# Performance work log

Hardware: AMD Instinct MI355X
Metric: run time of the kernel (lower is better)

The kernel has to match this reference:

```python
import jax, jax.numpy as jnp
import numpy as np

B, DIN, E, FACTOR, STEPS, NH = 2048, 1024, 1024, 16, 3, 8
DH = E // NH
EPS = 1e-5


def layernorm(x, g, b):
    m = x.mean(-1, keepdims=True)
    v = ((x - m) ** 2).mean(-1, keepdims=True)
    return (x - m) / jnp.sqrt(v + EPS) * g + b


def setup_inputs() -> dict:
    key = jax.random.key(0)
    ks = iter(jax.random.split(key, 32))
    r = lambda shape, s=0.02: jax.random.normal(next(ks), shape, dtype=jnp.float32) * s
    F = E * FACTOR
    return {
        "image_feat": jax.random.normal(next(ks), (B, DIN), dtype=jnp.float32),
        "text_feat": jax.random.normal(next(ks), (B, DIN), dtype=jnp.float32),
        # fusion block
        "fc1_w": r((F, DIN)), "fc1_b": jnp.zeros((F,), jnp.float32),
        "fc2_w": r((F, DIN)), "fc2_b": jnp.zeros((F,), jnp.float32),
        "fc3_w": r((E, F)), "fc3_b": jnp.zeros((E,), jnp.float32),
        "ln_g": jnp.ones((E,), jnp.float32), "ln_b": jnp.zeros((E,), jnp.float32),
        # per-step MHA + FFN + norms, stacked over STEPS
        "Wqkv": r((STEPS, 3 * E, E)), "bqkv": jnp.zeros((STEPS, 3 * E), jnp.float32),
        "Wo": r((STEPS, E, E)), "bo": jnp.zeros((STEPS, E), jnp.float32),
        "W1": r((STEPS, E, E)), "b1": jnp.zeros((STEPS, E), jnp.float32),
        "W2": r((STEPS, E, E)), "b2": jnp.zeros((STEPS, E), jnp.float32),
        "n1_g": jnp.ones((STEPS, E), jnp.float32), "n1_b": jnp.zeros((STEPS, E), jnp.float32),
        "n2_g": jnp.ones((STEPS, E), jnp.float32), "n2_b": jnp.zeros((STEPS, E), jnp.float32),
        # output projection
        "Wout": r((DIN, E)), "bout": jnp.zeros((DIN,), jnp.float32),
    }


def mha_step(q, ctx, Wqkv, bqkv, Wo, bo):
    # q: [B,E] (query len 1), ctx: [B,L,E]
    Wq, Wk, Wv = Wqkv[:E], Wqkv[E:2 * E], Wqkv[2 * E:]
    bq, bk, bv = bqkv[:E], bqkv[E:2 * E], bqkv[2 * E:]
    L = ctx.shape[1]
    qh = (q @ Wq.T + bq).reshape(B, NH, DH)
    kh = (ctx @ Wk.T + bk).reshape(B, L, NH, DH)
    vh = (ctx @ Wv.T + bv).reshape(B, L, NH, DH)
    scores = jnp.einsum("bhd,blhd->bhl", qh, kh) / jnp.sqrt(jnp.float32(DH))
    attn = jax.nn.softmax(scores, axis=-1)
    out = jnp.einsum("bhl,blhd->bhd", attn, vh).reshape(B, E)
    return out @ Wo.T + bo


def reference(image_feat, text_feat, fc1_w, fc1_b, fc2_w, fc2_b, fc3_w, fc3_b,
              ln_g, ln_b, Wqkv, bqkv, Wo, bo, W1, b1, W2, b2,
              n1_g, n1_b, n2_g, n2_b, Wout, bout):
    # fusion block (dropout = identity in eval)
    fused = (image_feat @ fc1_w.T + fc1_b) * (text_feat @ fc2_w.T + fc2_b)
    fused = layernorm(fused @ fc3_w.T + fc3_b, ln_g, ln_b)  # [B,E]
    ctx = fused[:, None, :]  # [B,1,E]
    x = fused
    for i in range(STEPS):
        attn = mha_step(x, ctx, Wqkv[i], bqkv[i], Wo[i], bo[i])
        x = x + layernorm(attn, n1_g[i], n1_b[i])
        ffn = jax.nn.relu(x @ W1[i].T + b1[i]) @ W2[i].T + b2[i]
        x = x + layernorm(ffn, n2_g[i], n2_b[i])
        ctx = jnp.concatenate([ctx, x[:, None, :]], axis=1)
    final_output = x @ Wout.T + bout  # [B,DIN]
    return final_output, ctx
```

## Files before the change

### kernel.cpp

```cpp
#include <hip/hip_runtime.h>

#define TB 256

typedef __attribute__((ext_vector_type(8))) short short8;
typedef __attribute__((ext_vector_type(4))) float f32x4;
typedef unsigned short u16;

constexpr int B_  = 2048;
constexpr int DIN = 1024;
constexpr int E   = 1024;
constexpr int F   = 16384;
constexpr int E3  = 3072;
constexpr int CH  = 4096;

struct Ptr8 { void* p[8]; };

__device__ __forceinline__ u16 f2bf(float f) {
  union { float f; unsigned u; } v; v.f = f;
  unsigned r = v.u + 0x7fffu + ((v.u >> 16) & 1u);
  return (u16)(r >> 16);
}
__device__ __forceinline__ float bf2f(u16 u) {
  union { unsigned u; float f; } v; v.u = ((unsigned)u) << 16;
  return v.f;
}

__device__ __forceinline__ void gload16(const void* g, void* l) {
  __builtin_amdgcn_global_load_lds(
      (const __attribute__((address_space(1))) void*)g,
      (__attribute__((address_space(3))) void*)l, 16, 0, 0);
}

__device__ __forceinline__ void tile_xy(int& tx, int& ty) {
  int gx = gridDim.x;
  int nwg = gx * gridDim.y;
  int wg = blockIdx.y * gx + blockIdx.x;
  if ((nwg & 7) == 0) wg = (wg & 7) * (nwg >> 3) + (wg >> 3);
  tx = wg % gx; ty = wg / gx;
}

__device__ __forceinline__ int swz16(int o) {
  return o ^ (((o >> 7) & 7) << 4);
}

__global__ __launch_bounds__(256) void cvt_kernel(const float* __restrict__ s,
                                                  u16* __restrict__ d, int n) {
  int i = (blockIdx.x * 256 + threadIdx.x) * 4;
  if (i >= n) return;
  float4 v = *(const float4*)&s[i];
  ushort4 o;
  o.x = f2bf(v.x); o.y = f2bf(v.y); o.z = f2bf(v.z); o.w = f2bf(v.w);
  *(ushort4*)&d[i] = o;
}

__global__ __launch_bounds__(256) void fill_kernel(float* p, int n, float v) {
  int i = blockIdx.x * 256 + threadIdx.x;
  if (i < n) p[i] = v;
}

__global__ __launch_bounds__(256) void relu_multi_kernel(
    Ptr8 ys, int ny, const float* __restrict__ bias, u16* __restrict__ out) {
  size_t i = ((size_t)blockIdx.x * 256 + threadIdx.x) * 4;
  int col = (int)(i & 1023);
  float4 b = *(const float4*)&bias[col];
  float a0 = b.x, a1 = b.y, a2 = b.z, a3 = b.w;
  for (int j = 0; j < ny; ++j) {
    float4 z = *(const float4*)&((const float*)ys.p[j])[i];
    a0 += z.x; a1 += z.y; a2 += z.z; a3 += z.w;
  }
  ushort4 o;
  o.x = f2bf(a0 > 0.f ? a0 : 0.f);
  o.y = f2bf(a1 > 0.f ? a1 : 0.f);
  o.z = f2bf(a2 > 0.f ? a2 : 0.f);
  o.w = f2bf(a3 > 0.f ? a3 : 0.f);
  *(ushort4*)&out[i] = o;
}

__global__ __launch_bounds__(256) void combine_out_kernel(
    Ptr8 ys, int ny, const float* __restrict__ bias, float* __restrict__ out) {
  size_t i = ((size_t)blockIdx.x * 256 + threadIdx.x) * 4;
  int col = (int)(i & 1023);
  float4 b = *(const float4*)&bias[col];
  float a0 = b.x, a1 = b.y, a2 = b.z, a3 = b.w;
  for (int j = 0; j < ny; ++j) {
    float4 z = *(const float4*)&((const float*)ys.p[j])[i];
    a0 += z.x; a1 += z.y; a2 += z.z; a3 += z.w;
  }
  out[i] = a0; out[i + 1] = a1; out[i + 2] = a2; out[i + 3] = a3;
}

template <int EPI>
__global__ __launch_bounds__(512, 2) void gemm256(
    const u16* __restrict__ A, int sA,
    const u16* __restrict__ Bw, int sB,
    const float* __restrict__ bias, const u16* __restrict__ gate,
    void* __restrict__ Out, Ptr8 pouts, int ldOut, int ksz) {
  __shared__ __align__(16) char smem[131072];
  const int tid = threadIdx.x, lane = tid & 63, w = tid >> 6;
  const int wm = w >> 2, wn = w & 3;
  int tx, ty; tile_xy(tx, ty);
  const int m0 = tx * 256, n0 = ty * 256;
  const int k0 = blockIdx.z * ksz;
  const int nt = ksz >> 6;
  const int lr = lane & 15;

  f32x4 acc[8][4] = {};

  auto stage = [&](const u16* __restrict__ G, int gs, int gr0, int kk, int tb, int j) {
    int P = j * 8192 + w * 1024 + lane * 16;
    int L = swz16(P);
    int row = L >> 7, colb = L & 127;
    gload16(G + (size_t)(gr0 + row) * gs + kk + (colb >> 1),
            &smem[tb + j * 8192 + w * 1024]);
  };
  auto rdA = [&](int tb, int mf, int kh) -> short8 {
    int Lo = (wm * 128 + mf * 16 + lr) * 128 + kh * 64 + (lane >> 4) * 16;
    return *(const short8*)&smem[tb + swz16(Lo)];
  };
  auto rdB = [&](int tb, int nf, int kh) -> short8 {
    int Lo = (wn * 64 + nf * 16 + lr) * 128 + kh * 64 + (lane >> 4) * 16;
    return *(const short8*)&smem[tb + swz16(Lo)];
  };

#pragma unroll
  for (int j = 0; j < 4; ++j) stage(A, sA, m0, k0, 0, j);
#pragma unroll
  for (int j = 0; j < 4; ++j) stage(Bw, sB, n0, k0, 65536, j);
  asm volatile("s_waitcnt vmcnt(0)" ::: "memory");
  __builtin_amdgcn_sched_barrier(0);
  __builtin_amdgcn_s_barrier();

  int cur = 0;
  for (int t = 0; t < nt; ++t) {
    const int sa = cur * 32768;
    const int sb = 65536 + cur * 32768;
    if (t + 1 < nt) {
      const int sa2 = (cur ^ 1) * 32768;
      const int sb2 = 65536 + (cur ^ 1) * 32768;
#pragma unroll
      for (int j = 0; j < 4; ++j) stage(A, sA, m0, k0 + (t + 1) * 64, sa2, j);
#pragma unroll
      for (int j = 0; j < 4; ++j) stage(Bw, sB, n0, k0 + (t + 1) * 64, sb2, j);
    }
    short8 bfr[4][2], afr[4][2];
#pragma unroll
    for (int nf = 0; nf < 4; ++nf)
#pragma unroll
      for (int kh = 0; kh < 2; ++kh) bfr[nf][kh] = rdB(sb, nf, kh);
#pragma unroll
    for (int mf = 0; mf < 4; ++mf)
#pragma unroll
      for (int kh = 0; kh < 2; ++kh) afr[mf][kh] = rdA(sa, mf, kh);
    __builtin_amdgcn_s_setprio(1);
#pragma unroll
    for (int mf = 0; mf < 4; ++mf)
#pragma unroll
      for (int nf = 0; nf < 4; ++nf)
#pragma unroll
        for (int kh = 0; kh < 2; ++kh)
          acc[mf][nf] = __builtin_amdgcn_mfma_f32_16x16x32_bf16(
              afr[mf][kh], bfr[nf][kh], acc[mf][nf], 0, 0, 0);
    __builtin_amdgcn_s_setprio(0);
#pragma unroll
    for (int mf = 0; mf < 4; ++mf)
#pragma unroll
      for (int kh = 0; kh < 2; ++kh) afr[mf][kh] = rdA(sa, 4 + mf, kh);
    __builtin_amdgcn_s_setprio(1);
#pragma unroll
    for (int mf = 0; mf < 4; ++mf)
#pragma unroll
      for (int nf = 0; nf < 4; ++nf)
#pragma unroll
        for (int kh = 0; kh < 2; ++kh)
          acc[4 + mf][nf] = __builtin_amdgcn_mfma_f32_16x16x32_bf16(
              afr[mf][kh], bfr[nf][kh], acc[4 + mf][nf], 0, 0, 0);
    __builtin_amdgcn_s_setprio(0);
    if (t + 1 < nt) {
      asm volatile("s_waitcnt vmcnt(0)" ::: "memory");
      __builtin_amdgcn_sched_barrier(0);
      __builtin_amdgcn_s_barrier();
    }
    cur ^= 1;
  }

  float* Pf = (EPI == 0) ? (float*)pouts.p[blockIdx.z] : nullptr;
  const int rb = (lane >> 4) * 4;
#pragma unroll
  for (int mf = 0; mf < 8; ++mf) {
#pragma unroll
    for (int nf = 0; nf < 4; ++nf) {
      int row0 = m0 + wm * 128 + mf * 16 + rb;
      int col  = n0 + wn * 64 + nf * 16 + lr;
      float bv = (EPI == 0 || bias == nullptr) ? 0.f : bias[col];
#pragma unroll
      for (int r = 0; r < 4; ++r) {
        float v = acc[mf][nf][r] + bv;
        size_t idx = (size_t)(row0 + r) * ldOut + col;
        if (EPI == 0)      Pf[idx] = v;
        else if (EPI == 4) ((u16*)Out)[idx] = f2bf(v * bf2f(gate[idx]));
        else               ((u16*)Out)[idx] = f2bf(v);
      }
    }
  }
}

template <int EPI>
__global__ __launch_bounds__(TB) void gemm_bt(
    const u16* __restrict__ A, int sA,
    const u16* __restrict__ Bw, int sB,
    const float* __restrict__ bias, Ptr8 outs,
    int ldOut, int Kext, int ksz) {
  __shared__ u16 As[128 * 32];
  __shared__ u16 Bs[128 * 32];
  const int tid = threadIdx.x, lane = tid & 63, w = tid >> 6;
  const int wr = w >> 1, wc = w & 1;
  int tx, ty; tile_xy(tx, ty);
  const int m0 = tx * 128, n0 = ty * 128;
  const int k0 = blockIdx.z * ksz;
  const int kend = min(k0 + ksz, Kext);

  f32x4 acc[4][4] = {};
  const int lr = lane & 15, lk = (lane >> 4) * 8;

  for (int kk = k0; kk < kend; kk += 32) {
#pragma unroll
    for (int is = 0; is < 2; ++is) {
      int c = is * 256 + tid;
      int r = c >> 2, kc = (c & 3) << 3;
      size_t lb = (size_t)(is * 256 + w * 64) * 8;
      gload16(A  + (size_t)(m0 + r) * sA + kk + kc, &As[lb]);
      gload16(Bw + (size_t)(n0 + r) * sB + kk + kc, &Bs[lb]);
    }
    __syncthreads();
    short8 af[4], bfv[4];
#pragma unroll
    for (int m = 0; m < 4; ++m)
      af[m] = *(const short8*)&As[(wr * 64 + m * 16 + lr) * 32 + lk];
#pragma unroll
    for (int n = 0; n < 4; ++n)
      bfv[n] = *(const short8*)&Bs[(wc * 64 + n * 16 + lr) * 32 + lk];
#pragma unroll
    for (int m = 0; m < 4; ++m)
#pragma unroll
      for (int n = 0; n < 4; ++n)
        acc[m][n] = __builtin_amdgcn_mfma_f32_16x16x32_bf16(af[m], bfv[n], acc[m][n], 0, 0, 0);
    __syncthreads();
  }

  float* Of = (float*)outs.p[EPI == 0 ? blockIdx.z : 0];
  const int rbase = (lane >> 4) * 4;
#pragma unroll
  for (int m = 0; m < 4; ++m) {
#pragma unroll
    for (int n = 0; n < 4; ++n) {
      int row0 = m0 + wr * 64 + m * 16 + rbase;
      int col  = n0 + wc * 64 + n * 16 + lr;
      float bv = (bias == nullptr) ? 0.f : bias[col];
#pragma unroll
      for (int r = 0; r < 4; ++r) {
        float v = acc[m][n][r] + bv;
        size_t idx = (size_t)(row0 + r) * ldOut + col;
        if (EPI == 0) Of[idx] = v;
        else          ((u16*)Of)[idx] = f2bf(v);
      }
    }
  }
}

template <int EPI>
__global__ __launch_bounds__(TB) void gemm_wf32(
    const u16* __restrict__ A, int sA,
    const float* __restrict__ Bw, int sB,
    const float* __restrict__ bias, void* __restrict__ Out, int ldOut,
    int Kext, int ksz) {
  __shared__ u16 As[128 * 32];
  __shared__ u16 Bs[128 * 32];
  const int tid = threadIdx.x, lane = tid & 63, w = tid >> 6;
  const int wr = w >> 1, wc = w & 1;
  int tx, ty; tile_xy(tx, ty);
  const int m0 = tx * 128, n0 = ty * 128;
  const int k0 = blockIdx.z * ksz;
  const int kend = min(k0 + ksz, Kext);

  f32x4 acc[4][4] = {};
  const int lr = lane & 15, lk = (lane >> 4) * 8;

  for (int kk = k0; kk < kend; kk += 32) {
#pragma unroll
    for (int is = 0; is < 2; ++is) {
      int c = is * 256 + tid;
      int r = c >> 2, kc = (c & 3) << 3;
      gload16(A + (size_t)(m0 + r) * sA + kk + kc,
              &As[(size_t)(is * 256 + w * 64) * 8]);
    }
#pragma unroll
    for (int p = 0; p < 4; ++p) {
      int t = tid + p * 256;
      int r = t >> 3, c4 = (t & 7) << 2;
      float4 v = *(const float4*)&Bw[(size_t)(n0 + r) * sB + kk + c4];
      ushort4 o;
      o.x = f2bf(v.x); o.y = f2bf(v.y); o.z = f2bf(v.z); o.w = f2bf(v.w);
      *(ushort4*)&Bs[r * 32 + c4] = o;
    }
    __syncthreads();
    short8 af[4], bfv[4];
#pragma unroll
    for (int m = 0; m < 4; ++m)
      af[m] = *(const short8*)&As[(wr * 64 + m * 16 + lr) * 32 + lk];
#pragma unroll
    for (int n = 0; n < 4; ++n)
      bfv[n] = *(const short8*)&Bs[(wc * 64 + n * 16 + lr) * 32 + lk];
#pragma unroll
    for (int m = 0; m < 4; ++m)
#pragma unroll
      for (int n = 0; n < 4; ++n)
        acc[m][n] = __builtin_amdgcn_mfma_f32_16x16x32_bf16(af[m], bfv[n], acc[m][n], 0, 0, 0);
    __syncthreads();
  }

  const int rbase = (lane >> 4) * 4;
#pragma unroll
  for (int m = 0; m < 4; ++m) {
#pragma unroll
    for (int n = 0; n < 4; ++n) {
      int row0 = m0 + wr * 64 + m * 16 + rbase;
      int col  = n0 + wc * 64 + n * 16 + lr;
      float bv = (EPI == 3 || bias == nullptr) ? 0.f : bias[col];
#pragma unroll
      for (int r = 0; r < 4; ++r) {
        float v = acc[m][n][r] + bv;
        size_t idx = (size_t)(row0 + r) * ldOut + col;
        if (EPI == 0)      ((float*)Out)[idx] = v;
        else if (EPI == 1) ((u16*)Out)[idx] = f2bf(v);
        else if (EPI == 2) ((u16*)Out)[idx] = f2bf(v > 0.f ? v : 0.f);
        else               atomicAdd((float*)Out + idx, v);
      }
    }
  }
}

__global__ __launch_bounds__(TB) void gemm_dual_wf32(
    const u16* __restrict__ A1, const u16* __restrict__ A2, int sA,
    const float* __restrict__ B1, const float* __restrict__ B2, int sB,
    const float* __restrict__ bias1, const float* __restrict__ bias2,
    u16* __restrict__ Out, int ldOut, int K) {
  __shared__ u16 As1[128 * 32];
  __shared__ u16 As2[128 * 32];
  __shared__ u16 Bs1[128 * 32];
  __shared__ u16 Bs2[128 * 32];
  const int tid = threadIdx.x, lane = tid & 63, w = tid >> 6;
  const int wr = w >> 1, wc = w & 1;
  int tx, ty; tile_xy(tx, ty);
  const int m0 = tx * 128, n0 = ty * 128;

  f32x4 acc1[4][4] = {};
  f32x4 acc2[4][4] = {};
  const int lr = lane & 15, lk = (lane >> 4) * 8;

  for (int kk = 0; kk < K; kk += 32) {
#pragma unroll
    for (int is = 0; is < 2; ++is) {
      int c = is * 256 + tid;
      int r = c >> 2, kc = (c & 3) << 3;
      size_t lb = (size_t)(is * 256 + w * 64) * 8;
      gload16(A1 + (size_t)(m0 + r) * sA + kk + kc, &As1[lb]);
      gload16(A2 + (size_t)(m0 + r) * sA + kk + kc, &As2[lb]);
    }
#pragma unroll
    for (int p = 0; p < 4; ++p) {
      int t = tid + p * 256;
      int r = t >> 3, c4 = (t & 7) << 2;
      float4 v1 = *(const float4*)&B1[(size_t)(n0 + r) * sB + kk + c4];
      float4 v2 = *(const float4*)&B2[(size_t)(n0 + r) * sB + kk + c4];
      ushort4 o1, o2;
      o1.x = f2bf(v1.x); o1.y = f2bf(v1.y); o1.z = f2bf(v1.z); o1.w = f2bf(v1.w);
      o2.x = f2bf(v2.x); o2.y = f2bf(v2.y); o2.z = f2bf(v2.z); o2.w = f2bf(v2.w);
      *(ushort4*)&Bs1[r * 32 + c4] = o1;
      *(ushort4*)&Bs2[r * 32 + c4] = o2;
    }
    __syncthreads();
    short8 a1[4], a2[4], b1v[4], b2v[4];
#pragma unroll
    for (int m = 0; m < 4; ++m) {
      a1[m] = *(const short8*)&As1[(wr * 64 + m * 16 + lr) * 32 + lk];
      a2[m] = *(const short8*)&As2[(wr * 64 + m * 16 + lr) * 32 + lk];
    }
#pragma unroll
    for (int n = 0; n < 4; ++n) {
      b1v[n] = *(const short8*)&Bs1[(wc * 64 + n * 16 + lr) * 32 + lk];
      b2v[n] = *(const short8*)&Bs2[(wc * 64 + n * 16 + lr) * 32 + lk];
    }
#pragma unroll
    for (int m = 0; m < 4; ++m)
#pragma unroll
      for (int n = 0; n < 4; ++n) {
        acc1[m][n] = __builtin_amdgcn_mfma_f32_16x16x32_bf16(a1[m], b1v[n], acc1[m][n], 0, 0, 0);
        acc2[m][n] = __builtin_amdgcn_mfma_f32_16x16x32_bf16(a2[m], b2v[n], acc2[m][n], 0, 0, 0);
      }
    __syncthreads();
  }

  const int rbase = (lane >> 4) * 4;
#pragma unroll
  for (int m = 0; m < 4; ++m) {
#pragma unroll
    for (int n = 0; n < 4; ++n) {
      int row0 = m0 + wr * 64 + m * 16 + rbase;
      int col  = n0 + wc * 64 + n * 16 + lr;
      float bv1 = bias1[col], bv2 = bias2[col];
#pragma unroll
      for (int r = 0; r < 4; ++r) {
        float v = (acc1[m][n][r] + bv1) * (acc2[m][n][r] + bv2);
        Out[(size_t)(row0 + r) * ldOut + col] = f2bf(v);
      }
    }
  }
}

template <int MODE>
__global__ __launch_bounds__(256) void resln_kernel(
    Ptr8 ys, int ny, const float* __restrict__ preb,
    const float* __restrict__ g, const float* __restrict__ bp,
    float* __restrict__ x, u16* __restrict__ xb,
    float* __restrict__ ctxo, int ctxRow) {
  const int r = blockIdx.x, tid = threadIdx.x;
  const size_t base = (size_t)r * 1024 + tid * 4;
  float y[4] = {0.f, 0.f, 0.f, 0.f};
  for (int j = 0; j < ny; ++j) {
    float4 z = *(const float4*)&((const float*)ys.p[j])[base];
    y[0] += z.x; y[1] += z.y; y[2] += z.z; y[3] += z.w;
  }
  if (preb != nullptr) {
    float4 p4 = *(const float4*)&preb[tid * 4];
    y[0] += p4.x; y[1] += p4.y; y[2] += p4.z; y[3] += p4.w;
  }
  float s = y[0] + y[1] + y[2] + y[3];
  float q = y[0] * y[0] + y[1] * y[1] + y[2] * y[2] + y[3] * y[3];
  __shared__ float red[8];
  for (int o = 32; o; o >>= 1) { s += __shfl_xor(s, o); q += __shfl_xor(q, o); }
  int wv = tid >> 6;
  if ((tid & 63) == 0) { red[wv] = s; red[4 + wv] = q; }
  __syncthreads();
  s = red[0] + red[1] + red[2] + red[3];
  q = red[4] + red[5] + red[6] + red[7];
  float mean = s * (1.f / 1024.f);
  float var  = q * (1.f / 1024.f) - mean * mean;
  float rs   = rsqrtf(var + 1e-5f);
  float4 g4 = *(const float4*)&g[tid * 4];
  float4 b4 = *(const float4*)&bp[tid * 4];
  float gg[4] = {g4.x, g4.y, g4.z, g4.w};
  float bb[4] = {b4.x, b4.y, b4.z, b4.w};
  float xv[4];
#pragma unroll
  for (int j = 0; j < 4; ++j) {
    float val = (y[j] - mean) * rs * gg[j] + bb[j];
    xv[j] = (MODE == 0) ? val : x[base + j] + val;
  }
  *(float4*)&x[base] = make_float4(xv[0], xv[1], xv[2], xv[3]);
  ushort4 xo;
  xo.x = f2bf(xv[0]); xo.y = f2bf(xv[1]); xo.z = f2bf(xv[2]); xo.w = f2bf(xv[3]);
  *(ushort4*)&xb[base] = xo;
  if (MODE != 1) {
    size_t cb = ((size_t)r * 4 + ctxRow) * 1024 + tid * 4;
    *(float4*)&ctxo[cb] = make_float4(xv[0], xv[1], xv[2], xv[3]);
  }
}

__global__ __launch_bounds__(64) void attn_kernel(const u16* __restrict__ qkv,
                                                  u16* __restrict__ out, int L) {
  const int b = blockIdx.x >> 3, h = blockIdx.x & 7;
  const int lane = threadIdx.x;
  const size_t qoff = ((size_t)(L - 1) * B_ + b) * E3 + h * 128;
  float q0 = bf2f(qkv[qoff + lane]);
  float q1 = bf2f(qkv[qoff + 64 + lane]);
  float sc[3];
  for (int l = 0; l < L; ++l) {
    size_t kb = ((size_t)l * B_ + b) * E3 + 1024 + h * 128;
    float p = q0 * bf2f(qkv[kb + lane]) + q1 * bf2f(qkv[kb + 64 + lane]);
    for (int o = 32; o; o >>= 1) p += __shfl_xor(p, o);
    sc[l] = p * 0.08838834764831843f;
  }
  float m = sc[0];
  for (int l = 1; l < L; ++l) m = fmaxf(m, sc[l]);
  float wsum = 0.f, wgt[3];
  for (int l = 0; l < L; ++l) { wgt[l] = expf(sc[l] - m); wsum += wgt[l]; }
  float inv = 1.f / wsum;
  float o0 = 0.f, o1 = 0.f;
  for (int l = 0; l < L; ++l) {
    size_t vb = ((size_t)l * B_ + b) * E3 + 2048 + h * 128;
    o0 += wgt[l] * bf2f(qkv[vb + lane]);
    o1 += wgt[l] * bf2f(qkv[vb + 64 + lane]);
  }
  out[(size_t)b * 1024 + h * 128 + lane]      = f2bf(o0 * inv);
  out[(size_t)b * 1024 + h * 128 + 64 + lane] = f2bf(o1 * inv);
}

extern "C" void kernel_launch(void* const* d_in, const int* in_sizes, int n_in,
                              void* d_out, int out_size, void* d_ws, size_t ws_size,
                              hipStream_t stream) {
  (void)in_sizes; (void)n_in;
  const float* image = (const float*)d_in[0];
  const float* text  = (const float*)d_in[1];
  const float* fc1_w = (const float*)d_in[2];
  const float* fc1_b = (const float*)d_in[3];
  const float* fc2_w = (const float*)d_in[4];
  const float* fc2_b = (const float*)d_in[5];
  const float* fc3_w = (const float*)d_in[6];
  const float* fc3_b = (const float*)d_in[7];
  const float* ln_g  = (const float*)d_in[8];
  const float* ln_b  = (const float*)d_in[9];
  const float* Wqkv  = (const float*)d_in[10];
  const float* bqkv  = (const float*)d_in[11];
  const float* Wo    = (const float*)d_in[12];
  const float* bo    = (const float*)d_in[13];
  const float* W1    = (const float*)d_in[14];
  const float* b1    = (const float*)d_in[15];
  const float* W2    = (const float*)d_in[16];
  const float* b2    = (const float*)d_in[17];
  const float* n1_g  = (const float*)d_in[18];
  const float* n1_b  = (const float*)d_in[19];
  const float* n2_g  = (const float*)d_in[20];
  const float* n2_b  = (const float*)d_in[21];
  const float* WoutW = (const float*)d_in[22];
  const float* boutW = (const float*)d_in[23];

  float* outF   = (float*)d_out;
  float* ctxOut = outF + (size_t)B_ * DIN;
  char* ws = (char*)d_ws;

  auto cvt = [&](const float* s, u16* d, size_t n) {
    cvt_kernel<<<dim3((unsigned)((n + 1023) / 1024)), 256, 0, stream>>>(s, d, (int)n);
  };

  const size_t NEED_A = 232783872;
  if (ws_size >= NEED_A) {
    size_t off = 0;
    auto carve = [&](size_t bytes) -> char* {
      char* p = ws + off; off += (bytes + 255) & ~(size_t)255; return p;
    };
    u16* imgB  = (u16*)carve((size_t)B_ * DIN * 2);
    u16* txtB  = (u16*)carve((size_t)B_ * DIN * 2);
    u16* fc1B  = (u16*)carve((size_t)F * DIN * 2);
    u16* fc2B  = (u16*)carve((size_t)F * DIN * 2);
    u16* fc3B  = (u16*)carve((size_t)E * F * 2);
    u16* WqkvB = (u16*)carve((size_t)3 * E3 * E * 2);
    u16* WoB   = (u16*)carve((size_t)3 * E * E * 2);
    u16* W1B   = (u16*)carve((size_t)3 * E * E * 2);
    u16* W2B   = (u16*)carve((size_t)3 * E * E * 2);
    u16* WoutB = (u16*)carve((size_t)DIN * E * 2);
    char* U    = carve((size_t)B_ * F * 2);
    float* xF  = (float*)carve((size_t)B_ * E * 4);
    float* hF  = (float*)carve((size_t)B_ * E * 4);
    u16* fusedB = (u16*)U;
    u16* qkvB   = (u16*)(U);
    u16* ctxB   = (u16*)(U + 37748736);
    u16* attnB  = (u16*)(U + 37748736 + 16777216);
    u16* h1B    = (u16*)(U + 37748736 + 16777216 + 4194304);
    u16* xbB    = (u16*)(U + 37748736 + 16777216 + 8388608);
    float* PA = (float*)fc1B;
    float* PB = (float*)(fc1B + 4194304);
    float* PC = (float*)(fc1B + 8388608);
    float* PD = (float*)(fc1B + 12582912);
    float* PE = (float*)fc2B;
    float* PF = (float*)(fc2B + 4194304);
    float* PG = (float*)(fc2B + 8388608);

    cvt(image, imgB, (size_t)B_ * DIN);
    cvt(text,  txtB, (size_t)B_ * DIN);
    cvt(fc1_w, fc1B, (size_t)F * DIN);
    cvt(fc2_w, fc2B, (size_t)F * DIN);
    cvt(fc3_w, fc3B, (size_t)E * F);
    cvt(Wqkv,  WqkvB, (size_t)3 * E3 * E);
    cvt(Wo,    WoB,   (size_t)3 * E * E);
    cvt(W1,    W1B,   (size_t)3 * E * E);
    cvt(W2,    W2B,   (size_t)3 * E * E);
    cvt(WoutW, WoutB, (size_t)DIN * E);

    Ptr8 dumb{};
    gemm256<1><<<dim3(B_ / 256, F / 256), 512, 0, stream>>>(
        txtB, DIN, fc2B, DIN, fc2_b, nullptr, fusedB, dumb, F, DIN);
    gemm256<4><<<dim3(B_ / 256, F / 256), 512, 0, stream>>>(
        imgB, DIN, fc1B, DIN, fc1_b, fusedB, fusedB, dumb, F, DIN);
    Ptr8 p8f{{xF, hF, PA, PB, PC, PD, PE, PF}};
    gemm256<0><<<dim3(B_ / 256, E / 256, 8), 512, 0, stream>>>(
        fusedB, F, fc3B, F, nullptr, nullptr, nullptr, p8f, E, F / 8);
    resln_kernel<0><<<B_, 256, 0, stream>>>(
        p8f, 8, fc3_b, ln_g, ln_b, xF, ctxB, ctxOut, 0);

    Ptr8 p8l{{hF, outF, PA, PB, PC, PD, PE, PF}};
    for (int i = 0; i < 3; ++i) {
      int L = i + 1;
      Ptr8 q1{{qkvB, nullptr, nullptr, nullptr, nullptr, nullptr, nullptr, nullptr}};
      gemm_bt<1><<<dim3(L * B_ / 128, E3 / 128), TB, 0, stream>>>(
          ctxB, E, WqkvB + (size_t)i * E3 * E, E, bqkv + (size_t)i * E3,
          q1, E3, E, E);
      attn_kernel<<<B_ * 8, 64, 0, stream>>>(qkvB, attnB, L);
      gemm_bt<0><<<dim3(B_ / 128, E / 128, 8), TB, 0, stream>>>(
          attnB, E, WoB + (size_t)i * E * E, E, nullptr, p8l, E, E, E / 8);
      resln_kernel<1><<<B_, 256, 0, stream>>>(
          p8l, 8, bo + (size_t)i * E, n1_g + (size_t)i * E, n1_b + (size_t)i * E,
          xF, xbB, nullptr, 0);
      gemm_bt<0><<<dim3(B_ / 128, E / 128, 8), TB, 0, stream>>>(
          xbB, E, W1B + (size_t)i * E * E, E, nullptr, p8l, E, E, E / 8);
      relu_multi_kernel<<<B_ * E / 1024, 256, 0, stream>>>(
          p8l, 8, b1 + (size_t)i * E, h1B);
      gemm_bt<0><<<dim3(B_ / 128, E / 128, 8), TB, 0, stream>>>(
          h1B, E, W2B + (size_t)i * E * E, E, nullptr, p8l, E, E, E / 8);
      resln_kernel<2><<<B_, 256, 0, stream>>>(
          p8l, 8, b2 + (size_t)i * E, n2_g + (size_t)i * E, n2_b + (size_t)i * E,
          xF, ctxB + (size_t)(i + 1) * B_ * E, ctxOut, i + 1);
    }

    Ptr8 pfin{{hF, PA, PB, PC, PD, PE, PF, PG}};
    gemm_bt<0><<<dim3(B_ / 128, DIN / 128, 8), TB, 0, stream>>>(
        ctxB + (size_t)3 * B_ * E, E, WoutB, E, nullptr, pfin, DIN, E, E / 8);
    combine_out_kernel<<<B_ * DIN / 1024, 256, 0, stream>>>(pfin, 8, boutW, outF);
    return;
  }

  size_t off = 0;
  auto carve = [&](size_t bytes) -> char* {
    char* p = ws + off; off += (bytes + 255) & ~(size_t)255; return p;
  };
  u16* imgB   = (u16*)carve((size_t)B_ * DIN * 2);
  u16* txtB   = (u16*)carve((size_t)B_ * DIN * 2);
  u16* fusedC = (u16*)carve((size_t)B_ * CH * 2);
  u16* qkvB   = (u16*)carve((size_t)3 * B_ * E3 * 2);
  u16* ctxB   = (u16*)carve((size_t)4 * B_ * E * 2);
  u16* attnB  = (u16*)carve((size_t)B_ * E * 2);
  u16* h1B    = (u16*)carve((size_t)B_ * E * 2);
  u16* xbB    = (u16*)carve((size_t)B_ * E * 2);
  float* xF   = (float*)carve((size_t)B_ * E * 4);
  float* hF   = (float*)carve((size_t)B_ * E * 4);

  if (off > ws_size) {
    fill_kernel<<<(out_size + 255) / 256, 256, 0, stream>>>(outF, out_size, 12345.0f);
    return;
  }

  cvt(image, imgB, (size_t)B_ * DIN);
  cvt(text,  txtB, (size_t)B_ * DIN);
  hipMemsetAsync(hF, 0, (size_t)B_ * E * 4, stream);

  for (int c = 0; c < F / CH; ++c) {
    gemm_dual_wf32<<<dim3(B_ / 128, CH / 128), TB, 0, stream>>>(
        imgB, txtB, DIN,
        fc1_w + (size_t)c * CH * DIN, fc2_w + (size_t)c * CH * DIN, DIN,
        fc1_b + (size_t)c * CH, fc2_b + (size_t)c * CH, fusedC, CH, DIN);
    gemm_wf32<3><<<dim3(B_ / 128, E / 128, 2), TB, 0, stream>>>(
        fusedC, CH, fc3_w + (size_t)c * CH, F, nullptr, hF, E, CH, CH / 2);
  }
  {
    Ptr8 y1{{hF, nullptr, nullptr, nullptr, nullptr, nullptr, nullptr, nullptr}};
    resln_kernel<0><<<B_, 256, 0, stream>>>(y1, 1, fc3_b, ln_g, ln_b, xF, ctxB, ctxOut, 0);
  }

  for (int i = 0; i < 3; ++i) {
    int L = i + 1;
    gemm_wf32<1><<<dim3(L * B_ / 128, E3 / 128), TB, 0, stream>>>(
        ctxB, E, Wqkv + (size_t)i * E3 * E, E, bqkv + (size_t)i * E3, qkvB, E3, E, E);
    attn_kernel<<<B_ * 8, 64, 0, stream>>>(qkvB, attnB, L);
    gemm_wf32<0><<<dim3(B_ / 128, E / 128), TB, 0, stream>>>(
        attnB, E, Wo + (size_t)i * E * E, E, bo + (size_t)i * E, hF, E, E, E);
    Ptr8 y1{{hF, nullptr, nullptr, nullptr, nullptr, nullptr, nullptr, nullptr}};
    resln_kernel<1><<<B_, 256, 0, stream>>>(
        y1, 1, nullptr, n1_g + (size_t)i * E, n1_b + (size_t)i * E, xF, xbB, nullptr, 0);
    gemm_wf32<2><<<dim3(B_ / 128, E / 128), TB, 0, stream>>>(
        xbB, E, W1 + (size_t)i * E * E, E, b1 + (size_t)i * E, h1B, E, E, E);
    gemm_wf32<0><<<dim3(B_ / 128, E / 128), TB, 0, stream>>>(
        h1B, E, W2 + (size_t)i * E * E, E, b2 + (size_t)i * E, hF, E, E, E);
    resln_kernel<2><<<B_, 256, 0, stream>>>(
        y1, 1, nullptr, n2_g + (size_t)i * E, n2_b + (size_t)i * E, xF,
        ctxB + (size_t)(i + 1) * B_ * E, ctxOut, i + 1);
  }
  gemm_wf32<0><<<dim3(B_ / 128, DIN / 128), TB, 0, stream>>>(
      ctxB + (size_t)3 * B_ * E, E, WoutW, E, boutW, outF, DIN, E, E);
}
```

Before: 910.1 us.

## Compute Q only for last context row, stage bf16 epilogue through LDS, halve split-K

The QKV projection previously computed Q, K and V for all L context rows, although only the last row's query is used. It now runs a K/V GEMM over all rows and a separate Q GEMM over the newest row only, cutting redundant projection FLOPs. The bf16 epilogue of gemm256 now stages each accumulator tile through LDS with a swizzle so it can write 16-byte vectorized global stores (including the gated variant). Split-K for the step GEMMs drops from 8 to 4, which reduces partial-sum traffic at the cost of fewer blocks.

```diff
diff --git a/kernel.cpp b/kernel.cpp
--- a/kernel.cpp
+++ b/kernel.cpp
@@ -183,22 +183,59 @@
     cur ^= 1;
   }
 
-  float* Pf = (EPI == 0) ? (float*)pouts.p[blockIdx.z] : nullptr;
-  const int rb = (lane >> 4) * 4;
-#pragma unroll
-  for (int mf = 0; mf < 8; ++mf) {
-#pragma unroll
-    for (int nf = 0; nf < 4; ++nf) {
-      int row0 = m0 + wm * 128 + mf * 16 + rb;
-      int col  = n0 + wn * 64 + nf * 16 + lr;
-      float bv = (EPI == 0 || bias == nullptr) ? 0.f : bias[col];
-#pragma unroll
-      for (int r = 0; r < 4; ++r) {
-        float v = acc[mf][nf][r] + bv;
-        size_t idx = (size_t)(row0 + r) * ldOut + col;
-        if (EPI == 0)      Pf[idx] = v;
-        else if (EPI == 4) ((u16*)Out)[idx] = f2bf(v * bf2f(gate[idx]));
-        else               ((u16*)Out)[idx] = f2bf(v);
+  if (EPI == 0) {
+    float* Pf = (float*)pouts.p[blockIdx.z];
+    const int rb = (lane >> 4) * 4;
+#pragma unroll
+    for (int mf = 0; mf < 8; ++mf) {
+#pragma unroll
+      for (int nf = 0; nf < 4; ++nf) {
+        int row0 = m0 + wm * 128 + mf * 16 + rb;
+        int col  = n0 + wn * 64 + nf * 16 + lr;
+#pragma unroll
+        for (int r = 0; r < 4; ++r)
+          Pf[(size_t)(row0 + r) * ldOut + col] = acc[mf][nf][r];
+      }
+    }
+  } else {
+    __syncthreads();
+    char* wbase = smem + w * 16384;
+    const int rb = (lane >> 4) * 4;
+    const int g4 = lane >> 4;
+#pragma unroll
+    for (int mf = 0; mf < 8; ++mf) {
+      char* wmf = wbase + mf * 2048;
+#pragma unroll
+      for (int nf = 0; nf < 4; ++nf) {
+        float bv = (bias == nullptr) ? 0.f : bias[n0 + wn * 64 + nf * 16 + lr];
+        int pb = nf ^ g4;
+#pragma unroll
+        for (int r = 0; r < 4; ++r)
+          *(u16*)&wmf[(rb + r) * 128 + pb * 32 + lr * 2] =
+              f2bf(acc[mf][nf][r] + bv);
+      }
+      asm volatile("s_waitcnt lgkmcnt(0)" ::: "memory");
+      __builtin_amdgcn_sched_barrier(0);
+      int rrow = lane >> 2, wb = lane & 3;
+      int pb2 = wb ^ (rrow >> 2);
+      short8 v0 = *(const short8*)&wmf[rrow * 128 + pb2 * 32];
+      short8 v1 = *(const short8*)&wmf[rrow * 128 + pb2 * 32 + 16];
+      size_t gidx = (size_t)(m0 + wm * 128 + mf * 16 + rrow) * ldOut +
+                    (n0 + wn * 64 + wb * 16);
+      if (EPI == 4) {
+        short8 g0 = *(const short8*)&gate[gidx];
+        short8 g1 = *(const short8*)&gate[gidx + 8];
+        short8 o0, o1;
+#pragma unroll
+        for (int j = 0; j < 8; ++j) {
+          o0[j] = (short)f2bf(bf2f((u16)v0[j]) * bf2f((u16)g0[j]));
+          o1[j] = (short)f2bf(bf2f((u16)v1[j]) * bf2f((u16)g1[j]));
+        }
+        *(short8*)((u16*)Out + gidx) = o0;
+        *(short8*)((u16*)Out + gidx + 8) = o1;
+      } else {
+        *(short8*)((u16*)Out + gidx) = v0;
+        *(short8*)((u16*)Out + gidx + 8) = v1;
       }
     }
   }
@@ -466,17 +503,19 @@
   }
 }
 
-__global__ __launch_bounds__(64) void attn_kernel(const u16* __restrict__ qkv,
-                                                  u16* __restrict__ out, int L) {
+__global__ __launch_bounds__(64) void attn_kernel(
+    const u16* __restrict__ q, int qstride,
+    const u16* __restrict__ kv, int kvstride, int voff,
+    u16* __restrict__ out, int L) {
   const int b = blockIdx.x >> 3, h = blockIdx.x & 7;
   const int lane = threadIdx.x;
-  const size_t qoff = ((size_t)(L - 1) * B_ + b) * E3 + h * 128;
-  float q0 = bf2f(qkv[qoff + lane]);
-  float q1 = bf2f(qkv[qoff + 64 + lane]);
+  const size_t qoff = (size_t)b * qstride + h * 128;
+  float q0 = bf2f(q[qoff + lane]);
+  float q1 = bf2f(q[qoff + 64 + lane]);
   float sc[3];
   for (int l = 0; l < L; ++l) {
-    size_t kb = ((size_t)l * B_ + b) * E3 + 1024 + h * 128;
-    float p = q0 * bf2f(qkv[kb + lane]) + q1 * bf2f(qkv[kb + 64 + lane]);
+    size_t kb = ((size_t)l * B_ + b) * kvstride + h * 128;
+    float p = q0 * bf2f(kv[kb + lane]) + q1 * bf2f(kv[kb + 64 + lane]);
     for (int o = 32; o; o >>= 1) p += __shfl_xor(p, o);
     sc[l] = p * 0.08838834764831843f;
   }
@@ -487,9 +526,9 @@
   float inv = 1.f / wsum;
   float o0 = 0.f, o1 = 0.f;
   for (int l = 0; l < L; ++l) {
-    size_t vb = ((size_t)l * B_ + b) * E3 + 2048 + h * 128;
-    o0 += wgt[l] * bf2f(qkv[vb + lane]);
-    o1 += wgt[l] * bf2f(qkv[vb + 64 + lane]);
+    size_t vb = ((size_t)l * B_ + b) * kvstride + voff + h * 128;
+    o0 += wgt[l] * bf2f(kv[vb + lane]);
+    o1 += wgt[l] * bf2f(kv[vb + 64 + lane]);
   }
   out[(size_t)b * 1024 + h * 128 + lane]      = f2bf(o0 * inv);
   out[(size_t)b * 1024 + h * 128 + 64 + lane] = f2bf(o1 * inv);
@@ -552,7 +591,8 @@
     float* xF  = (float*)carve((size_t)B_ * E * 4);
     float* hF  = (float*)carve((size_t)B_ * E * 4);
     u16* fusedB = (u16*)U;
-    u16* qkvB   = (u16*)(U);
+    u16* kvB    = (u16*)(U);
+    u16* qB     = (u16*)(U + 25165824);
     u16* ctxB   = (u16*)(U + 37748736);
     u16* attnB  = (u16*)(U + 37748736 + 16777216);
     u16* h1B    = (u16*)(U + 37748736 + 16777216 + 4194304);
@@ -563,7 +603,6 @@
     float* PD = (float*)(fc1B + 12582912);
     float* PE = (float*)fc2B;
     float* PF = (float*)(fc2B + 4194304);
-    float* PG = (float*)(fc2B + 8388608);
 
     cvt(image, imgB, (size_t)B_ * DIN);
     cvt(text,  txtB, (size_t)B_ * DIN);
@@ -587,34 +626,38 @@
     resln_kernel<0><<<B_, 256, 0, stream>>>(
         p8f, 8, fc3_b, ln_g, ln_b, xF, ctxB, ctxOut, 0);
 
-    Ptr8 p8l{{hF, outF, PA, PB, PC, PD, PE, PF}};
+    Ptr8 p4{{hF, outF, PA, PB, nullptr, nullptr, nullptr, nullptr}};
     for (int i = 0; i < 3; ++i) {
       int L = i + 1;
-      Ptr8 q1{{qkvB, nullptr, nullptr, nullptr, nullptr, nullptr, nullptr, nullptr}};
-      gemm_bt<1><<<dim3(L * B_ / 128, E3 / 128), TB, 0, stream>>>(
-          ctxB, E, WqkvB + (size_t)i * E3 * E, E, bqkv + (size_t)i * E3,
-          q1, E3, E, E);
-      attn_kernel<<<B_ * 8, 64, 0, stream>>>(qkvB, attnB, L);
-      gemm_bt<0><<<dim3(B_ / 128, E / 128, 8), TB, 0, stream>>>(
-          attnB, E, WoB + (size_t)i * E * E, E, nullptr, p8l, E, E, E / 8);
+      Ptr8 qkv1{{kvB, nullptr, nullptr, nullptr, nullptr, nullptr, nullptr, nullptr}};
+      gemm_bt<1><<<dim3(L * B_ / 128, 2 * E / 128), TB, 0, stream>>>(
+          ctxB, E, WqkvB + (size_t)i * E3 * E + (size_t)E * E, E,
+          bqkv + (size_t)i * E3 + E, qkv1, 2 * E, E, E);
+      Ptr8 qkv2{{qB, nullptr, nullptr, nullptr, nullptr, nullptr, nullptr, nullptr}};
+      gemm_bt<1><<<dim3(B_ / 128, E / 128), TB, 0, stream>>>(
+          ctxB + (size_t)i * B_ * E, E, WqkvB + (size_t)i * E3 * E, E,
+          bqkv + (size_t)i * E3, qkv2, E, E, E);
+      attn_kernel<<<B_ * 8, 64, 0, stream>>>(qB, E, kvB, 2 * E, E, attnB, L);
+      gemm_bt<0><<<dim3(B_ / 128, E / 128, 4), TB, 0, stream>>>(
+          attnB, E, WoB + (size_t)i * E * E, E, nullptr, p4, E, E, E / 4);
       resln_kernel<1><<<B_, 256, 0, stream>>>(
-          p8l, 8, bo + (size_t)i * E, n1_g + (size_t)i * E, n1_b + (size_t)i * E,
+          p4, 4, bo + (size_t)i * E, n1_g + (size_t)i * E, n1_b + (size_t)i * E,
           xF, xbB, nullptr, 0);
-      gemm_bt<0><<<dim3(B_ / 128, E / 128, 8), TB, 0, stream>>>(
-          xbB, E, W1B + (size_t)i * E * E, E, nullptr, p8l, E, E, E / 8);
+      gemm_bt<0><<<dim3(B_ / 128, E / 128, 4), TB, 0, stream>>>(
+          xbB, E, W1B + (size_t)i * E * E, E, nullptr, p4, E, E, E / 4);
       relu_multi_kernel<<<B_ * E / 1024, 256, 0, stream>>>(
-          p8l, 8, b1 + (size_t)i * E, h1B);
-      gemm_bt<0><<<dim3(B_ / 128, E / 128, 8), TB, 0, stream>>>(
-          h1B, E, W2B + (size_t)i * E * E, E, nullptr, p8l, E, E, E / 8);
+          p4, 4, b1 + (size_t)i * E, h1B);
+      gemm_bt<0><<<dim3(B_ / 128, E / 128, 4), TB, 0, stream>>>(
+          h1B, E, W2B + (size_t)i * E * E, E, nullptr, p4, E, E, E / 4);
       resln_kernel<2><<<B_, 256, 0, stream>>>(
-          p8l, 8, b2 + (size_t)i * E, n2_g + (size_t)i * E, n2_b + (size_t)i * E,
+          p4, 4, b2 + (size_t)i * E, n2_g + (size_t)i * E, n2_b + (size_t)i * E,
           xF, ctxB + (size_t)(i + 1) * B_ * E, ctxOut, i + 1);
     }
 
-    Ptr8 pfin{{hF, PA, PB, PC, PD, PE, PF, PG}};
-    gemm_bt<0><<<dim3(B_ / 128, DIN / 128, 8), TB, 0, stream>>>(
-        ctxB + (size_t)3 * B_ * E, E, WoutB, E, nullptr, pfin, DIN, E, E / 8);
-    combine_out_kernel<<<B_ * DIN / 1024, 256, 0, stream>>>(pfin, 8, boutW, outF);
+    Ptr8 pfin{{hF, PA, PB, PC, nullptr, nullptr, nullptr, nullptr}};
+    gemm_bt<0><<<dim3(B_ / 128, DIN / 128, 4), TB, 0, stream>>>(
+        ctxB + (size_t)3 * B_ * E, E, WoutB, E, nullptr, pfin, DIN, E, E / 4);
+    combine_out_kernel<<<B_ * DIN / 1024, 256, 0, stream>>>(pfin, 4, boutW, outF);
     return;
   }
 
@@ -659,7 +702,8 @@
     int L = i + 1;
     gemm_wf32<1><<<dim3(L * B_ / 128, E3 / 128), TB, 0, stream>>>(
         ctxB, E, Wqkv + (size_t)i * E3 * E, E, bqkv + (size_t)i * E3, qkvB, E3, E, E);
-    attn_kernel<<<B_ * 8, 64, 0, stream>>>(qkvB, attnB, L);
+    attn_kernel<<<B_ * 8, 64, 0, stream>>>(
+        qkvB + (size_t)(L - 1) * B_ * E3, E3, qkvB + 1024, E3, 1024, attnB, L);
     gemm_wf32<0><<<dim3(B_ / 128, E / 128), TB, 0, stream>>>(
         attnB, E, Wo + (size_t)i * E * E, E, bo + (size_t)i * E, hF, E, E, E);
     Ptr8 y1{{hF, nullptr, nullptr, nullptr, nullptr, nullptr, nullptr, nullptr}};
```

New measurement: 836.6 us. 8.1% less time.
